# Kernel tuning notes

Hardware: AMD Instinct MI355X
Metric: run time of the kernel (lower is better)

Reference implementation:

```python
import jax, jax.numpy as jnp
import numpy as np

THRESHOLDS = (0.25, 0.375, 0.5, 0.625)
NUM_CLASSES = 5
SMOOTH = 1e-5  # dice smoothing constant


def setup_inputs() -> dict:
    key = jax.random.key(0)
    k1, k2 = jax.random.split(key)
    # [N, T, C, H, W]; input has 5 class channels, target 1 intensity channel
    inp = jax.random.uniform(k1, (4, 10, 5, 384, 384), dtype=jnp.float32)
    tgt = jax.random.uniform(k2, (4, 10, 1, 384, 384), dtype=jnp.float32)
    weight = jnp.array([1.0, 1.0, 2.0, 5.0, 10.0], dtype=jnp.float32)
    return {"input": inp, "target": tgt, "weight": weight}


def reference(input, target, weight):
    # permute to [N, C, T, H, W]
    x = jnp.transpose(input, (0, 2, 1, 3, 4))   # [N,5,T,H,W]
    t = jnp.transpose(target, (0, 2, 1, 3, 4))  # [N,1,T,H,W]
    # threshold binning: class index = number of thresholds <= target value
    cls = jnp.zeros(t.shape, dtype=jnp.int32)
    for thr in THRESHOLDS:
        cls = cls + (t >= thr).astype(jnp.int32)
    # one-hot scatter along class dim -> [N,5,T,H,W]
    class_ids = jnp.arange(NUM_CLASSES, dtype=jnp.int32).reshape(1, NUM_CLASSES, 1, 1, 1)
    onehot = (cls == class_ids).astype(x.dtype)
    # per-class dice over all remaining dims
    axes = (0, 2, 3, 4)
    inter = jnp.sum(x * onehot, axis=axes)                      # [5]
    denom = jnp.sum(x, axis=axes) + jnp.sum(onehot, axis=axes)  # [5]
    dice_loss = 1.0 - (2.0 * inter + SMOOTH) / (denom + SMOOTH)  # [5]
    return jnp.sum(weight * dice_loss)
```

## Files before the change

kernel.cpp:

```cpp
#include <hip/hip_runtime.h>

#define HW      147456
#define NC      5
#define NT      40
#define NPIX    (NT * HW)
#define NGROUP  (NPIX / 4)
#define SMOOTH  1e-5f

__global__ void dice_init_ws(float* __restrict__ ws) {
    if (threadIdx.x < 16) ws[threadIdx.x] = 0.0f;
}

__global__ __launch_bounds__(256) void dice_main(const float* __restrict__ inp,
                                                 const float* __restrict__ tgt,
                                                 float* __restrict__ ws) {
    float sumx[NC]  = {0.f, 0.f, 0.f, 0.f, 0.f};
    float inter[NC] = {0.f, 0.f, 0.f, 0.f, 0.f};
    float cnt[NC]   = {0.f, 0.f, 0.f, 0.f, 0.f};

    const int tid    = blockIdx.x * 256 + threadIdx.x;
    const int stride = gridDim.x * 256;

    for (int g = tid; g < NGROUP; g += stride) {
        const int p  = g << 2;
        const int nt = p / HW;
        const int hw = p - nt * HW;

        const float4 t4 = reinterpret_cast<const float4*>(tgt)[g];
        const int c0 = (t4.x >= 0.25f) + (t4.x >= 0.375f) + (t4.x >= 0.5f) + (t4.x >= 0.625f);
        const int c1 = (t4.y >= 0.25f) + (t4.y >= 0.375f) + (t4.y >= 0.5f) + (t4.y >= 0.625f);
        const int c2 = (t4.z >= 0.25f) + (t4.z >= 0.375f) + (t4.z >= 0.5f) + (t4.z >= 0.625f);
        const int c3 = (t4.w >= 0.25f) + (t4.w >= 0.375f) + (t4.w >= 0.5f) + (t4.w >= 0.625f);

        const float* base = inp + (size_t)nt * (size_t)(NC * HW) + (size_t)hw;
        #pragma unroll
        for (int c = 0; c < NC; ++c) {
            const float4 x4 = *reinterpret_cast<const float4*>(base + (size_t)c * HW);
            sumx[c] += (x4.x + x4.y) + (x4.z + x4.w);
            float iv = 0.f;
            if (c0 == c) iv += x4.x;
            if (c1 == c) iv += x4.y;
            if (c2 == c) iv += x4.z;
            if (c3 == c) iv += x4.w;
            inter[c] += iv;
            cnt[c]   += (float)((c0 == c) + (c1 == c) + (c2 == c) + (c3 == c));
        }
    }

    float v[15];
    #pragma unroll
    for (int c = 0; c < NC; ++c) { v[c] = sumx[c]; v[5 + c] = inter[c]; v[10 + c] = cnt[c]; }

    #pragma unroll
    for (int j = 0; j < 15; ++j) {
        #pragma unroll
        for (int off = 32; off > 0; off >>= 1)
            v[j] += __shfl_down(v[j], off, 64);
    }

    __shared__ float part[4][15];
    const int lane = threadIdx.x & 63;
    const int wv   = threadIdx.x >> 6;
    if (lane == 0) {
        #pragma unroll
        for (int j = 0; j < 15; ++j) part[wv][j] = v[j];
    }
    __syncthreads();
    if (threadIdx.x < 15) {
        const float s = part[0][threadIdx.x] + part[1][threadIdx.x] +
                        part[2][threadIdx.x] + part[3][threadIdx.x];
        atomicAdd(&ws[threadIdx.x], s);
    }
}

__global__ void dice_final(const float* __restrict__ ws,
                           const float* __restrict__ w,
                           float* __restrict__ out) {
    if (threadIdx.x == 0) {
        float loss = 0.f;
        #pragma unroll
        for (int c = 0; c < NC; ++c) {
            const float inter = ws[5 + c];
            const float denom = ws[c] + ws[10 + c];
            loss += w[c] * (1.f - (2.f * inter + SMOOTH) / (denom + SMOOTH));
        }
        out[0] = loss;
    }
}

extern "C" void kernel_launch(void* const* d_in, const int* in_sizes, int n_in,
                              void* d_out, int out_size, void* d_ws, size_t ws_size,
                              hipStream_t stream) {
    const float* inp = (const float*)d_in[0];
    const float* tgt = (const float*)d_in[1];
    const float* wgt = (const float*)d_in[2];
    float* out = (float*)d_out;
    float* ws  = (float*)d_ws;

    dice_init_ws<<<1, 64, 0, stream>>>(ws);
    dice_main<<<1440, 256, 0, stream>>>(inp, tgt, ws);
    dice_final<<<1, 64, 0, stream>>>(ws, wgt, out);
}
```

Before: 195.7 us.

## Use 2D grid per slice, write per-block partials, drop init kernel and atomics

The main kernel now runs on a 2D grid with one y-row per (n,t) slice and a fixed two-iteration loop, which removes the per-element integer division. Each block writes its 15 partial sums to its own slot in the workspace instead of using atomicAdd. The final kernel uses 960 threads to reduce the 2880 partials per quantity. With no accumulator to zero, the init kernel is gone, saving a launch. The kernel is memory-bound over about 141 MB, so most of the time is DRAM traffic and launch and atomic savings are small.

```diff
diff --git a/kernel.cpp b/kernel.cpp
--- a/kernel.cpp
+++ b/kernel.cpp
@@ -3,36 +3,37 @@
 #define HW      147456
 #define NC      5
 #define NT      40
-#define NPIX    (NT * HW)
-#define NGROUP  (NPIX / 4)
+#define GPS     36864
+#define BX      72
+#define TPS     (BX * 256)
+#define NBLK    (BX * NT)
 #define SMOOTH  1e-5f
 
-__global__ void dice_init_ws(float* __restrict__ ws) {
-    if (threadIdx.x < 16) ws[threadIdx.x] = 0.0f;
-}
 
 __global__ __launch_bounds__(256) void dice_main(const float* __restrict__ inp,
                                                  const float* __restrict__ tgt,
                                                  float* __restrict__ ws) {
+    const int nt = blockIdx.y;
+    const int t0 = blockIdx.x * 256 + threadIdx.x;
+
+    const float* __restrict__ tb = tgt + (size_t)nt * (size_t)HW;
+    const float* __restrict__ ib = inp + (size_t)nt * (size_t)(NC * HW);
+
     float sumx[NC]  = {0.f, 0.f, 0.f, 0.f, 0.f};
     float inter[NC] = {0.f, 0.f, 0.f, 0.f, 0.f};
     float cnt[NC]   = {0.f, 0.f, 0.f, 0.f, 0.f};
 
-    const int tid    = blockIdx.x * 256 + threadIdx.x;
-    const int stride = gridDim.x * 256;
+    #pragma unroll
+    for (int it = 0; it < 2; ++it) {
+        const int g = t0 + it * TPS;
+        const float4 t4 = reinterpret_cast<const float4*>(tb)[g];
 
-    for (int g = tid; g < NGROUP; g += stride) {
-        const int p  = g << 2;
-        const int nt = p / HW;
-        const int hw = p - nt * HW;
-
-        const float4 t4 = reinterpret_cast<const float4*>(tgt)[g];
         const int c0 = (t4.x >= 0.25f) + (t4.x >= 0.375f) + (t4.x >= 0.5f) + (t4.x >= 0.625f);
         const int c1 = (t4.y >= 0.25f) + (t4.y >= 0.375f) + (t4.y >= 0.5f) + (t4.y >= 0.625f);
         const int c2 = (t4.z >= 0.25f) + (t4.z >= 0.375f) + (t4.z >= 0.5f) + (t4.z >= 0.625f);
         const int c3 = (t4.w >= 0.25f) + (t4.w >= 0.375f) + (t4.w >= 0.5f) + (t4.w >= 0.625f);
 
-        const float* base = inp + (size_t)nt * (size_t)(NC * HW) + (size_t)hw;
+        const float* base = ib + ((size_t)g << 2);
         #pragma unroll
         for (int c = 0; c < NC; ++c) {
             const float4 x4 = *reinterpret_cast<const float4*>(base + (size_t)c * HW);
@@ -69,19 +70,34 @@
     if (threadIdx.x < 15) {
         const float s = part[0][threadIdx.x] + part[1][threadIdx.x] +
                         part[2][threadIdx.x] + part[3][threadIdx.x];
-        atomicAdd(&ws[threadIdx.x], s);
+        ws[threadIdx.x * NBLK + (blockIdx.y * BX + blockIdx.x)] = s;
     }
 }
 
-__global__ void dice_final(const float* __restrict__ ws,
-                           const float* __restrict__ w,
-                           float* __restrict__ out) {
+__global__ __launch_bounds__(960) void dice_final(const float* __restrict__ ws,
+                                                  const float* __restrict__ w,
+                                                  float* __restrict__ out) {
+    __shared__ float red[15];
+    const int j    = threadIdx.x >> 6;
+    const int lane = threadIdx.x & 63;
+
+    float s = 0.f;
+    for (int b = lane; b < NBLK; b += 64)
+        s += ws[j * NBLK + b];
+
+    #pragma unroll
+    for (int off = 32; off > 0; off >>= 1)
+        s += __shfl_down(s, off, 64);
+
+    if (lane == 0) red[j] = s;
+    __syncthreads();
+
     if (threadIdx.x == 0) {
         float loss = 0.f;
         #pragma unroll
         for (int c = 0; c < NC; ++c) {
-            const float inter = ws[5 + c];
-            const float denom = ws[c] + ws[10 + c];
+            const float inter = red[5 + c];
+            const float denom = red[c] + red[10 + c];
             loss += w[c] * (1.f - (2.f * inter + SMOOTH) / (denom + SMOOTH));
         }
         out[0] = loss;
@@ -97,7 +113,6 @@
     float* out = (float*)d_out;
     float* ws  = (float*)d_ws;
 
-    dice_init_ws<<<1, 64, 0, stream>>>(ws);
-    dice_main<<<1440, 256, 0, stream>>>(inp, tgt, ws);
-    dice_final<<<1, 64, 0, stream>>>(ws, wgt, out);
+    dice_main<<<dim3(BX, NT), 256, 0, stream>>>(inp, tgt, ws);
+    dice_final<<<1, 960, 0, stream>>>(ws, wgt, out);
 }
```

Result: slower. 202.5 us (+3.5%).
